# Kernel tuning notes

Hardware: AMD Instinct MI355X
Metric: run time of the kernel (lower is better)

## Reference

```python
import jax, jax.numpy as jnp
import numpy as np

D_MODEL = 1024
NUM_HEADS = 16
D_K = D_MODEL // NUM_HEADS
LOCAL_WINDOW = 3
STRIDE = 4


def strided_mask(seq_len):
    # position i attends to j iff j <= i and (i-j <= local_window or (i-j) % stride == 0)
    i = jnp.arange(seq_len)[:, None]
    j = jnp.arange(seq_len)[None, :]
    d = i - j
    return (d >= 0) & ((d <= LOCAL_WINDOW) | (d % STRIDE == 0))


def setup_inputs() -> dict:
    key = jax.random.key(0)
    ks = jax.random.split(key, 11)
    B, S, D = 4, 1024, D_MODEL
    s = 1.0 / np.sqrt(D)
    inp = {
        "Q": jax.random.normal(ks[0], (B, S, D), jnp.float32),
        "K": jax.random.normal(ks[1], (B, S, D), jnp.float32),
        "V": jax.random.normal(ks[2], (B, S, D), jnp.float32),
        "Wq": jax.random.normal(ks[3], (D, D), jnp.float32) * s,
        "bq": jnp.zeros((D,), jnp.float32),
        "Wk": jax.random.normal(ks[4], (D, D), jnp.float32) * s,
        "bk": jnp.zeros((D,), jnp.float32),
        "Wv": jax.random.normal(ks[5], (D, D), jnp.float32) * s,
        "bv": jnp.zeros((D,), jnp.float32),
        "Wo": jax.random.normal(ks[6], (D, D), jnp.float32) * s,
        "bo": jnp.zeros((D,), jnp.float32),
    }
    return inp


def reference(Q, K, V, Wq, bq, Wk, bk, Wv, bv, Wo, bo):
    B, S, D = Q.shape
    H, dk = NUM_HEADS, D_K

    def split(x):  # [B,S,D] -> [B,H,S,dk]
        return x.reshape(B, S, H, dk).transpose(0, 2, 1, 3)

    q = split(Q @ Wq + bq)
    k = split(K @ Wk + bk)
    v = split(V @ Wv + bv)

    scores = jnp.einsum("bhsd,bhtd->bhst", q, k) / jnp.sqrt(
        jnp.asarray(dk, jnp.float32))
    m = strided_mask(S)[None, None]  # [1,1,S,S]
    scores = jnp.where(m, scores, -1e9)
    attn = jax.nn.softmax(scores, axis=-1)
    out = jnp.einsum("bhst,bhtd->bhsd", attn, v)
    out = out.transpose(0, 2, 1, 3).reshape(B, S, D)  # combine heads
    return out @ Wo + bo
```

## Files before the change

kernel.cpp:

```cpp
#include <hip/hip_runtime.h>

typedef _Float16 f16;
typedef __attribute__((ext_vector_type(8))) _Float16 f16x8;
typedef __attribute__((ext_vector_type(4))) _Float16 f16x4;
typedef __attribute__((ext_vector_type(4))) float f32x4;

#define MFMA16(a, b, c) __builtin_amdgcn_mfma_f32_16x16x32_f16((a), (b), (c), 0, 0, 0)

__device__ __forceinline__ void gld_lds16(const void* g, void* l) {
  __builtin_amdgcn_global_load_lds(
      (__attribute__((address_space(1))) void*)const_cast<void*>(g),
      (__attribute__((address_space(3))) void*)l, 16, 0, 0);
}

__device__ __forceinline__ f16x8 ld8(const f16* p) { return *(const f16x8*)p; }

__global__ __launch_bounds__(256) void cvt_all_kernel(
    const float* __restrict__ Q, const float* __restrict__ K, const float* __restrict__ V,
    f16* __restrict__ oq, f16* __restrict__ ok, f16* __restrict__ ov,
    const float* __restrict__ Wq, const float* __restrict__ Wk,
    const float* __restrict__ Wv, const float* __restrict__ Wo,
    f16* __restrict__ Tq, f16* __restrict__ Tk, f16* __restrict__ Tv, f16* __restrict__ To) {
  __shared__ float tile[64][65];
  if (blockIdx.z < 3) {
    const float* src = blockIdx.z == 0 ? Q : (blockIdx.z == 1 ? K : V);
    f16* dst = blockIdx.z == 0 ? oq : (blockIdx.z == 1 ? ok : ov);
    size_t i = ((size_t)blockIdx.x * 256 + threadIdx.x) * 4;
    float4 f = *(const float4*)(src + i);
    f16x4 o4;
    o4.x = (f16)f.x; o4.y = (f16)f.y; o4.z = (f16)f.z; o4.w = (f16)f.w;
    *(f16x4*)(dst + i) = o4;
    return;
  }
  if (blockIdx.x >= 1024) return;
  const int zz = blockIdx.x >> 8;
  const float* W = zz == 0 ? Wq : (zz == 1 ? Wk : (zz == 2 ? Wv : Wo));
  f16* T = zz == 0 ? Tq : (zz == 1 ? Tk : (zz == 2 ? Tv : To));
  const int tidx = blockIdx.x & 255;
  const int k0 = (tidx & 15) * 64, n0 = (tidx >> 4) * 64;
  const int tx = threadIdx.x & 63, ty = threadIdx.x >> 6;
#pragma unroll
  for (int rr = 0; rr < 16; ++rr) {
    int r = rr * 4 + ty;
    tile[r][tx] = W[(size_t)(k0 + r) * 1024 + n0 + tx];
  }
  __syncthreads();
#pragma unroll
  for (int rr = 0; rr < 16; ++rr) {
    int nn = rr * 4 + ty;
    T[(size_t)(n0 + nn) * 1024 + k0 + tx] = (f16)tile[tx][nn];
  }
}

template <bool QKV>
__global__ __launch_bounds__(256) void gemm_bt_kernel(
    const f16* __restrict__ A0, const f16* __restrict__ A1, const f16* __restrict__ A2,
    const f16* __restrict__ B0, const f16* __restrict__ B1, const f16* __restrict__ B2,
    const float* __restrict__ bias0, const float* __restrict__ bias1, const float* __restrict__ bias2,
    f16* __restrict__ C0, f16* __restrict__ C1, f16* __restrict__ C2,
    f16* __restrict__ C3, float* __restrict__ Cf) {
  const int z = blockIdx.z;
  const f16* A = z == 0 ? A0 : (z == 1 ? A1 : A2);
  const f16* Bt = z == 0 ? B0 : (z == 1 ? B1 : B2);
  const float* bias = z == 0 ? bias0 : (z == 1 ? bias1 : bias2);

  __shared__ alignas(16) f16 lA[128 * 64];
  __shared__ alignas(16) f16 lB[128 * 64];

  const int t = threadIdx.x;
  const int w = t >> 6, lane = t & 63, quad = lane >> 4, l15 = lane & 15;
  const int wm = w >> 1, wn = w & 1;
  const int mbase = blockIdx.x * 128;
  const int nbase = blockIdx.y * 128;

  const f32x4 zero4 = {0.f, 0.f, 0.f, 0.f};
  f32x4 acc[4][4];
#pragma unroll
  for (int mi = 0; mi < 4; ++mi)
#pragma unroll
    for (int ni = 0; ni < 4; ++ni) acc[mi][ni] = zero4;

  const int rsub = t >> 3;
  const int kswz = ((t & 7) ^ (rsub & 7)) << 3;

  for (int k0 = 0; k0 < 1024; k0 += 64) {
    __syncthreads();
#pragma unroll
    for (int c4 = 0; c4 < 4; ++c4) {
      gld_lds16(A + (size_t)(mbase + c4 * 32 + rsub) * 1024 + k0 + kswz,
                (char*)lA + c4 * 4096 + w * 1024);
      gld_lds16(Bt + (size_t)(nbase + c4 * 32 + rsub) * 1024 + k0 + kswz,
                (char*)lB + c4 * 4096 + w * 1024);
    }
    __syncthreads();

    f16x8 af[2][4], bf[2][4];
#pragma unroll
    for (int ko = 0; ko < 2; ++ko) {
      const int pos = (((ko << 2) | quad) ^ (l15 & 7)) << 3;
#pragma unroll
      for (int mi = 0; mi < 4; ++mi)
        af[ko][mi] = ld8(&lA[(wm * 64 + mi * 16 + l15) * 64 + pos]);
#pragma unroll
      for (int ni = 0; ni < 4; ++ni)
        bf[ko][ni] = ld8(&lB[(wn * 64 + ni * 16 + l15) * 64 + pos]);
    }
#pragma unroll
    for (int ko = 0; ko < 2; ++ko)
#pragma unroll
      for (int mi = 0; mi < 4; ++mi)
#pragma unroll
        for (int ni = 0; ni < 4; ++ni)
          acc[mi][ni] = MFMA16(af[ko][mi], bf[ko][ni], acc[mi][ni]);
  }

#pragma unroll
  for (int mi = 0; mi < 4; ++mi) {
#pragma unroll
    for (int ni = 0; ni < 4; ++ni) {
#pragma unroll
      for (int rg = 0; rg < 4; ++rg) {
        const int row = mbase + wm * 64 + mi * 16 + quad * 4 + rg;
        const int col = nbase + wn * 64 + ni * 16 + l15;
        const float v = acc[mi][ni][rg] + bias[col];
        if (QKV) {
          const int bh = (row >> 10) * 16 + (col >> 6);
          const int s = row & 1023, d = col & 63;
          const f16 hv = (f16)v;
          if (z != 2) {
            f16* Ch = (z == 0) ? C0 : C1;
            Ch[(size_t)bh * 65536 + s * 64 + d] = hv;
          } else {
            C2[(size_t)bh * 65536 + s * 64 + d] = hv;
            const int rr = s & 3, n = s >> 2, wi = n & 63;
            C3[(size_t)bh * 65536 + (size_t)rr * 16384 + (size_t)d * 256 +
               (n & ~63) + ((wi & 15) << 2) + (wi >> 4)] = hv;
          }
        } else {
          Cf[(size_t)row * 1024 + col] = v;
        }
      }
    }
  }
}

__global__ __launch_bounds__(256) void gemm_out_kernel(
    const f16* __restrict__ A, const f16* __restrict__ Bt,
    const float* __restrict__ bias, float* __restrict__ Cf) {
  __shared__ alignas(16) f16 lA[64 * 64];
  __shared__ alignas(16) f16 lB[128 * 64];

  const int t = threadIdx.x;
  const int w = t >> 6, lane = t & 63, quad = lane >> 4, l15 = lane & 15;
  const int wm = w >> 1, wn = w & 1;
  const int mbase = blockIdx.x * 64;
  const int nbase = blockIdx.y * 128;

  const f32x4 zero4 = {0.f, 0.f, 0.f, 0.f};
  f32x4 acc[2][4];
#pragma unroll
  for (int mi = 0; mi < 2; ++mi)
#pragma unroll
    for (int ni = 0; ni < 4; ++ni) acc[mi][ni] = zero4;

  const int rsub = t >> 3;
  const int kswz = ((t & 7) ^ (rsub & 7)) << 3;

  for (int k0 = 0; k0 < 1024; k0 += 64) {
    __syncthreads();
    gld_lds16(A + (size_t)(mbase + rsub) * 1024 + k0 + kswz, (char*)lA + w * 1024);
    gld_lds16(A + (size_t)(mbase + 32 + rsub) * 1024 + k0 + kswz, (char*)lA + 4096 + w * 1024);
#pragma unroll
    for (int c4 = 0; c4 < 4; ++c4)
      gld_lds16(Bt + (size_t)(nbase + c4 * 32 + rsub) * 1024 + k0 + kswz,
                (char*)lB + c4 * 4096 + w * 1024);
    __syncthreads();

    f16x8 af[2][2], bf[2][4];
#pragma unroll
    for (int ko = 0; ko < 2; ++ko) {
      const int pos = (((ko << 2) | quad) ^ (l15 & 7)) << 3;
#pragma unroll
      for (int mi = 0; mi < 2; ++mi)
        af[ko][mi] = ld8(&lA[(wm * 32 + mi * 16 + l15) * 64 + pos]);
#pragma unroll
      for (int ni = 0; ni < 4; ++ni)
        bf[ko][ni] = ld8(&lB[(wn * 64 + ni * 16 + l15) * 64 + pos]);
    }
#pragma unroll
    for (int ko = 0; ko < 2; ++ko)
#pragma unroll
      for (int mi = 0; mi < 2; ++mi)
#pragma unroll
        for (int ni = 0; ni < 4; ++ni)
          acc[mi][ni] = MFMA16(af[ko][mi], bf[ko][ni], acc[mi][ni]);
  }

#pragma unroll
  for (int mi = 0; mi < 2; ++mi)
#pragma unroll
    for (int ni = 0; ni < 4; ++ni)
#pragma unroll
      for (int rg = 0; rg < 4; ++rg) {
        const int row = mbase + wm * 32 + mi * 16 + quad * 4 + rg;
        const int col = nbase + wn * 64 + ni * 16 + l15;
        Cf[(size_t)row * 1024 + col] = acc[mi][ni][rg] + bias[col];
      }
}

__global__ __launch_bounds__(256) void attn_far_kernel(
    const f16* __restrict__ qh, const f16* __restrict__ kh,
    const f16* __restrict__ vtg, float* __restrict__ po, float* __restrict__ ml) {
  const int t = threadIdx.x;
  const int w = t >> 6, lane = t & 63, quad = lane >> 4, l15 = lane & 15;
  const int widx = blockIdx.x + 512 * w;
  const int bh = (widx & 255) >> 2, r = widx & 3;
  const int wq = widx >> 8;
  const int m0 = wq * 32;
  const int ntiles = (wq >> 1) + 1;

  __shared__ alignas(16) f16 lp[4][2][16 * 72];

  const f16* qb = qh + (size_t)bh * 65536;
  const f16* kb = kh + (size_t)bh * 65536;
  const f16* vb = vtg + (size_t)bh * 65536 + (size_t)r * 16384;
  const float SCL2 = 0.125f * 1.44269504f;

  f16x8 aq[2][2];
#pragma unroll
  for (int mt = 0; mt < 2; ++mt) {
    const int i = 4 * (m0 + mt * 16 + l15) + r;
#pragma unroll
    for (int ko = 0; ko < 2; ++ko)
      aq[mt][ko] = ld8(qb + (size_t)i * 64 + ko * 32 + quad * 8);
  }

  const f32x4 zero4 = {0.f, 0.f, 0.f, 0.f};
  f32x4 o[2][4];
  float mrun[2][4], lrun[2][4];
#pragma unroll
  for (int mt = 0; mt < 2; ++mt)
#pragma unroll
    for (int i = 0; i < 4; ++i) {
      o[mt][i] = zero4; mrun[mt][i] = -1e30f; lrun[mt][i] = 0.f;
    }

  for (int jt = 0; jt < ntiles; ++jt) {
    const int n0 = jt * 64;
    f16x8 bk0[4], bk1[4], bv0[4], bv1[4];
#pragma unroll
    for (int nt = 0; nt < 4; ++nt) {
      const f16* kr = kb + (size_t)(4 * (n0 + nt * 16 + l15) + r) * 64;
      bk0[nt] = ld8(kr + quad * 8);
      bk1[nt] = ld8(kr + 32 + quad * 8);
      const f16* vr = vb + (size_t)(nt * 16 + l15) * 256 + n0;
      bv0[nt] = ld8(vr + quad * 8);
      bv1[nt] = ld8(vr + 32 + quad * 8);
    }
    const bool lastt = (jt == ntiles - 1);
#pragma unroll
    for (int mt = 0; mt < 2; ++mt) {
      f32x4 sc[4];
#pragma unroll
      for (int nt = 0; nt < 4; ++nt) {
        f32x4 c = MFMA16(aq[mt][0], bk0[nt], zero4);
        sc[nt] = MFMA16(aq[mt][1], bk1[nt], c);
      }
#pragma unroll
      for (int rg = 0; rg < 4; ++rg) {
        const int m = m0 + mt * 16 + quad * 4 + rg;
        float s[4];
#pragma unroll
        for (int nt = 0; nt < 4; ++nt) {
          float vsc = sc[nt][rg] * SCL2;
          if (lastt) vsc = (n0 + nt * 16 + l15 <= m) ? vsc : -3.0e38f;
          s[nt] = vsc;
        }
        float tm = fmaxf(fmaxf(s[0], s[1]), fmaxf(s[2], s[3]));
        tm = fmaxf(tm, __shfl_xor(tm, 1));
        tm = fmaxf(tm, __shfl_xor(tm, 2));
        tm = fmaxf(tm, __shfl_xor(tm, 4));
        tm = fmaxf(tm, __shfl_xor(tm, 8));
        const float mnew = fmaxf(mrun[mt][rg], tm);
        const float alpha = exp2f(mrun[mt][rg] - mnew);
        float p[4], ps = 0.f;
#pragma unroll
        for (int nt = 0; nt < 4; ++nt) { p[nt] = exp2f(s[nt] - mnew); ps += p[nt]; }
        ps += __shfl_xor(ps, 1);
        ps += __shfl_xor(ps, 2);
        ps += __shfl_xor(ps, 4);
        ps += __shfl_xor(ps, 8);
        lrun[mt][rg] = lrun[mt][rg] * alpha + ps;
        mrun[mt][rg] = mnew;
#pragma unroll
        for (int ntv = 0; ntv < 4; ++ntv) o[mt][ntv][rg] *= alpha;
        f16x4 pk;
        pk.x = (f16)p[0]; pk.y = (f16)p[1]; pk.z = (f16)p[2]; pk.w = (f16)p[3];
        *(f16x4*)&lp[w][mt][(quad * 4 + rg) * 72 + l15 * 4] = pk;
      }
    }
#pragma unroll
    for (int mt = 0; mt < 2; ++mt) {
      const f16x8 ap0 = ld8(&lp[w][mt][l15 * 72 + quad * 8]);
      const f16x8 ap1 = ld8(&lp[w][mt][l15 * 72 + 32 + quad * 8]);
#pragma unroll
      for (int ntv = 0; ntv < 4; ++ntv) {
        f32x4 c = MFMA16(ap0, bv0[ntv], o[mt][ntv]);
        o[mt][ntv] = MFMA16(ap1, bv1[ntv], c);
      }
    }
  }

#pragma unroll
  for (int mt = 0; mt < 2; ++mt)
#pragma unroll
    for (int rg = 0; rg < 4; ++rg) {
      const int i = 4 * (m0 + mt * 16 + quad * 4 + rg) + r;
      const size_t idx = (size_t)bh * 1024 + i;
#pragma unroll
      for (int ntv = 0; ntv < 4; ++ntv)
        po[idx * 64 + ntv * 16 + l15] = o[mt][ntv][rg];
      if (l15 == 0) { ml[idx * 2] = mrun[mt][rg]; ml[idx * 2 + 1] = lrun[mt][rg]; }
    }
}

__global__ __launch_bounds__(256) void attn_diag_kernel(
    const f16* __restrict__ qh, const f16* __restrict__ kh, const f16* __restrict__ vh,
    const float* __restrict__ po, const float* __restrict__ ml, f16* __restrict__ ao) {
  const int t = threadIdx.x;
  const int widx = blockIdx.x * 4 + (t >> 6);
  const int l = t & 63;
  const int bh = widx >> 10, i = widx & 1023;
  const float SCL2 = 0.125f * 1.44269504f;

  const float q = (float)qh[(size_t)bh * 65536 + (size_t)i * 64 + l];
  float s[3];
#pragma unroll
  for (int d = 1; d <= 3; ++d) {
    const int j = i - d;
    const int jc = j < 0 ? 0 : j;
    float pr = q * (float)kh[(size_t)bh * 65536 + (size_t)jc * 64 + l];
    pr += __shfl_xor(pr, 1);
    pr += __shfl_xor(pr, 2);
    pr += __shfl_xor(pr, 4);
    pr += __shfl_xor(pr, 8);
    pr += __shfl_xor(pr, 16);
    pr += __shfl_xor(pr, 32);
    s[d - 1] = (j >= 0) ? pr * SCL2 : -3.0e38f;
  }
  const float md = fmaxf(fmaxf(s[0], s[1]), s[2]);
  const size_t idx = (size_t)bh * 1024 + i;
  const float mf = ml[idx * 2], lf = ml[idx * 2 + 1];
  const float M = fmaxf(md, mf);
  float p[3], ld = 0.f;
#pragma unroll
  for (int d = 1; d <= 3; ++d) { p[d - 1] = exp2f(s[d - 1] - M); ld += p[d - 1]; }
  float ov = 0.f;
#pragma unroll
  for (int d = 1; d <= 3; ++d) {
    const int jc = (i - d) < 0 ? 0 : (i - d);
    ov += p[d - 1] * (float)vh[(size_t)bh * 65536 + (size_t)jc * 64 + l];
  }
  const float fs = exp2f(mf - M);
  const float lt = lf * fs + ld;
  const float of = po[idx * 64 + l];
  const float res = (of * fs + ov) / lt;
  const int b = bh >> 4, h = bh & 15;
  ao[((size_t)(b * 1024 + i)) * 1024 + h * 64 + l] = (f16)res;
}

extern "C" void kernel_launch(void* const* d_in, const int* in_sizes, int n_in,
                              void* d_out, int out_size, void* d_ws, size_t ws_size,
                              hipStream_t stream) {
  const float* Q = (const float*)d_in[0];
  const float* K = (const float*)d_in[1];
  const float* V = (const float*)d_in[2];
  const float* Wq = (const float*)d_in[3];
  const float* bq = (const float*)d_in[4];
  const float* Wk = (const float*)d_in[5];
  const float* bk = (const float*)d_in[6];
  const float* Wv = (const float*)d_in[7];
  const float* bv = (const float*)d_in[8];
  const float* Wo = (const float*)d_in[9];
  const float* bo = (const float*)d_in[10];
  float* out = (float*)d_out;

  char* ws = (char*)d_ws;
  const size_t MB = 1ull << 20;
  f16* Xq  = (f16*)(ws + 0 * MB);
  f16* Xk  = (f16*)(ws + 8 * MB);
  f16* Xv  = (f16*)(ws + 16 * MB);
  f16* TWq = (f16*)(ws + 24 * MB);
  f16* TWk = (f16*)(ws + 26 * MB);
  f16* TWv = (f16*)(ws + 28 * MB);
  f16* TWo = (f16*)(ws + 30 * MB);
  f16* qhb = (f16*)(ws + 32 * MB);
  f16* khb = (f16*)(ws + 40 * MB);
  f16* vhb = (f16*)(ws + 48 * MB);
  f16* vtg = (f16*)(ws + 56 * MB);
  float* po  = (float*)(ws + 0 * MB);
  float* mlb = (float*)(ws + 16 * MB);
  f16* aob   = (f16*)(ws + 17 * MB);

  cvt_all_kernel<<<dim3(4096, 1, 4), 256, 0, stream>>>(
      Q, K, V, Xq, Xk, Xv, Wq, Wk, Wv, Wo, TWq, TWk, TWv, TWo);
  gemm_bt_kernel<true><<<dim3(32, 8, 3), 256, 0, stream>>>(
      Xq, Xk, Xv, TWq, TWk, TWv, bq, bk, bv, qhb, khb, vhb, vtg, nullptr);
  attn_far_kernel<<<dim3(512), 256, 0, stream>>>(qhb, khb, vtg, po, mlb);
  attn_diag_kernel<<<dim3(16384), 256, 0, stream>>>(qhb, khb, vhb, po, mlb, aob);
  gemm_out_kernel<<<dim3(64, 8), 256, 0, stream>>>(aob, TWo, bo, out);
}
```

Before: 229.5 us.

## Double-buffer LDS tiles in projection GEMMs with K=32 stages

```diff
diff --git a/kernel.cpp b/kernel.cpp
--- a/kernel.cpp
+++ b/kernel.cpp
@@ -64,8 +64,8 @@
   const f16* Bt = z == 0 ? B0 : (z == 1 ? B1 : B2);
   const float* bias = z == 0 ? bias0 : (z == 1 ? bias1 : bias2);
 
-  __shared__ alignas(16) f16 lA[128 * 64];
-  __shared__ alignas(16) f16 lB[128 * 64];
+  __shared__ alignas(16) f16 lA[2][128 * 32];
+  __shared__ alignas(16) f16 lB[2][128 * 32];
 
   const int t = threadIdx.x;
   const int w = t >> 6, lane = t & 63, quad = lane >> 4, l15 = lane & 15;
@@ -80,39 +80,43 @@
 #pragma unroll
     for (int ni = 0; ni < 4; ++ni) acc[mi][ni] = zero4;
 
-  const int rsub = t >> 3;
-  const int kswz = ((t & 7) ^ (rsub & 7)) << 3;
-
+  const int r = t >> 2;
+  const int koff = (t & 3) * 8;
+
+#define STAGE_BT(buf, k0)                                                               \
+  do {                                                                                  \
+    gld_lds16(A + (size_t)(mbase + r) * 1024 + (k0) + koff, (char*)lA[buf] + w * 1024); \
+    gld_lds16(A + (size_t)(mbase + 64 + r) * 1024 + (k0) + koff,                        \
+              (char*)lA[buf] + 4096 + w * 1024);                                        \
+    gld_lds16(Bt + (size_t)(nbase + r) * 1024 + (k0) + koff, (char*)lB[buf] + w * 1024);\
+    gld_lds16(Bt + (size_t)(nbase + 64 + r) * 1024 + (k0) + koff,                       \
+              (char*)lB[buf] + 4096 + w * 1024);                                        \
+  } while (0)
+
+#define COMPUTE_BT(buf)                                                     \
+  do {                                                                      \
+    f16x8 af[4], bf[4];                                                     \
+    _Pragma("unroll") for (int mi = 0; mi < 4; ++mi)                        \
+        af[mi] = ld8(&lA[buf][(wm * 64 + mi * 16 + l15) * 32 + quad * 8]);  \
+    _Pragma("unroll") for (int ni = 0; ni < 4; ++ni)                        \
+        bf[ni] = ld8(&lB[buf][(wn * 64 + ni * 16 + l15) * 32 + quad * 8]);  \
+    _Pragma("unroll") for (int mi = 0; mi < 4; ++mi)                        \
+        _Pragma("unroll") for (int ni = 0; ni < 4; ++ni)                    \
+            acc[mi][ni] = MFMA16(af[mi], bf[ni], acc[mi][ni]);              \
+  } while (0)
+
+  STAGE_BT(0, 0);
+  __syncthreads();
   for (int k0 = 0; k0 < 1024; k0 += 64) {
+    STAGE_BT(1, k0 + 32);
+    COMPUTE_BT(0);
     __syncthreads();
-#pragma unroll
-    for (int c4 = 0; c4 < 4; ++c4) {
-      gld_lds16(A + (size_t)(mbase + c4 * 32 + rsub) * 1024 + k0 + kswz,
-                (char*)lA + c4 * 4096 + w * 1024);
-      gld_lds16(Bt + (size_t)(nbase + c4 * 32 + rsub) * 1024 + k0 + kswz,
-                (char*)lB + c4 * 4096 + w * 1024);
-    }
+    if (k0 + 64 < 1024) STAGE_BT(0, k0 + 64);
+    COMPUTE_BT(1);
     __syncthreads();
-
-    f16x8 af[2][4], bf[2][4];
-#pragma unroll
-    for (int ko = 0; ko < 2; ++ko) {
-      const int pos = (((ko << 2) | quad) ^ (l15 & 7)) << 3;
-#pragma unroll
-      for (int mi = 0; mi < 4; ++mi)
-        af[ko][mi] = ld8(&lA[(wm * 64 + mi * 16 + l15) * 64 + pos]);
-#pragma unroll
-      for (int ni = 0; ni < 4; ++ni)
-        bf[ko][ni] = ld8(&lB[(wn * 64 + ni * 16 + l15) * 64 + pos]);
-    }
-#pragma unroll
-    for (int ko = 0; ko < 2; ++ko)
-#pragma unroll
-      for (int mi = 0; mi < 4; ++mi)
-#pragma unroll
-        for (int ni = 0; ni < 4; ++ni)
-          acc[mi][ni] = MFMA16(af[ko][mi], bf[ko][ni], acc[mi][ni]);
-  }
+  }
+#undef STAGE_BT
+#undef COMPUTE_BT
 
 #pragma unroll
   for (int mi = 0; mi < 4; ++mi) {
@@ -147,8 +151,8 @@
 __global__ __launch_bounds__(256) void gemm_out_kernel(
     const f16* __restrict__ A, const f16* __restrict__ Bt,
     const float* __restrict__ bias, float* __restrict__ Cf) {
-  __shared__ alignas(16) f16 lA[64 * 64];
-  __shared__ alignas(16) f16 lB[128 * 64];
+  __shared__ alignas(16) f16 lA[2][64 * 32];
+  __shared__ alignas(16) f16 lB[2][128 * 32];
 
   const int t = threadIdx.x;
   const int w = t >> 6, lane = t & 63, quad = lane >> 4, l15 = lane & 15;
@@ -163,38 +167,41 @@
 #pragma unroll
     for (int ni = 0; ni < 4; ++ni) acc[mi][ni] = zero4;
 
-  const int rsub = t >> 3;
-  const int kswz = ((t & 7) ^ (rsub & 7)) << 3;
-
+  const int r = t >> 2;
+  const int koff = (t & 3) * 8;
+
+#define STAGE_OUT(buf, k0)                                                              \
+  do {                                                                                  \
+    gld_lds16(A + (size_t)(mbase + r) * 1024 + (k0) + koff, (char*)lA[buf] + w * 1024); \
+    gld_lds16(Bt + (size_t)(nbase + r) * 1024 + (k0) + koff, (char*)lB[buf] + w * 1024);\
+    gld_lds16(Bt + (size_t)(nbase + 64 + r) * 1024 + (k0) + koff,                       \
+              (char*)lB[buf] + 4096 + w * 1024);                                        \
+  } while (0)
+
+#define COMPUTE_OUT(buf)                                                    \
+  do {                                                                      \
+    f16x8 af[2], bf[4];                                                     \
+    _Pragma("unroll") for (int mi = 0; mi < 2; ++mi)                        \
+        af[mi] = ld8(&lA[buf][(wm * 32 + mi * 16 + l15) * 32 + quad * 8]);  \
+    _Pragma("unroll") for (int ni = 0; ni < 4; ++ni)                        \
+        bf[ni] = ld8(&lB[buf][(wn * 64 + ni * 16 + l15) * 32 + quad * 8]);  \
+    _Pragma("unroll") for (int mi = 0; mi < 2; ++mi)                        \
+        _Pragma("unroll") for (int ni = 0; ni < 4; ++ni)                    \
+            acc[mi][ni] = MFMA16(af[mi], bf[ni], acc[mi][ni]);              \
+  } while (0)
+
+  STAGE_OUT(0, 0);
+  __syncthreads();
   for (int k0 = 0; k0 < 1024; k0 += 64) {
+    STAGE_OUT(1, k0 + 32);
+    COMPUTE_OUT(0);
     __syncthreads();
-    gld_lds16(A + (size_t)(mbase + rsub) * 1024 + k0 + kswz, (char*)lA + w * 1024);
-    gld_lds16(A + (size_t)(mbase + 32 + rsub) * 1024 + k0 + kswz, (char*)lA + 4096 + w * 1024);
-#pragma unroll
-    for (int c4 = 0; c4 < 4; ++c4)
-      gld_lds16(Bt + (size_t)(nbase + c4 * 32 + rsub) * 1024 + k0 + kswz,
-                (char*)lB + c4 * 4096 + w * 1024);
+    if (k0 + 64 < 1024) STAGE_OUT(0, k0 + 64);
+    COMPUTE_OUT(1);
     __syncthreads();
-
-    f16x8 af[2][2], bf[2][4];
-#pragma unroll
-    for (int ko = 0; ko < 2; ++ko) {
-      const int pos = (((ko << 2) | quad) ^ (l15 & 7)) << 3;
-#pragma unroll
-      for (int mi = 0; mi < 2; ++mi)
-        af[ko][mi] = ld8(&lA[(wm * 32 + mi * 16 + l15) * 64 + pos]);
-#pragma unroll
-      for (int ni = 0; ni < 4; ++ni)
-        bf[ko][ni] = ld8(&lB[(wn * 64 + ni * 16 + l15) * 64 + pos]);
-    }
-#pragma unroll
-    for (int ko = 0; ko < 2; ++ko)
-#pragma unroll
-      for (int mi = 0; mi < 2; ++mi)
-#pragma unroll
-        for (int ni = 0; ni < 4; ++ni)
-          acc[mi][ni] = MFMA16(af[ko][mi], bf[ko][ni], acc[mi][ni]);
-  }
+  }
+#undef STAGE_OUT
+#undef COMPUTE_OUT
 
 #pragma unroll
   for (int mi = 0; mi < 2; ++mi)
```

After: 241.2 us. 5.1% more time.
